# Performance work log

Measured on AMD Instinct MI355X. Metric: run time of the kernel, lower is better.

Reference implementation:

```python
import jax, jax.numpy as jnp
import numpy as np

B = 4          # number of prefill sequences (uniform cu_seqlens)
S = 1024       # tokens per sequence; total_tokens = B*S
SCALE = 0.08838834764831845  # head_dim ** -0.5


def setup_inputs() -> dict:
    key = jax.random.key(0)
    k1, k2, k3 = jax.random.split(key, 3)
    N, H, Hk, D = B * S, 16, 4, 128
    q = jax.random.normal(k1, (N, H, D), dtype=jnp.float32)
    k = jax.random.normal(k2, (N, Hk, D), dtype=jnp.float32)
    v = jax.random.normal(k3, (N, Hk, D), dtype=jnp.float32)
    k_cache = jnp.zeros((N, Hk * D), dtype=jnp.float32)
    v_cache = jnp.zeros((N, Hk * D), dtype=jnp.float32)
    slot_mapping = jnp.arange(N, dtype=jnp.int32)
    return {"q": q, "k": k, "v": v, "k_cache": k_cache,
            "v_cache": v_cache, "slot_mapping": slot_mapping}


def _store_kvcache(k, v, k_cache, v_cache, slot_mapping):
    # scatter token KV into flat paged cache; slot == -1 means skip
    N = k.shape[0]
    valid = slot_mapping >= 0
    slot = jnp.where(valid, slot_mapping, 0)
    k_flat = k.reshape(N, -1)
    v_flat = v.reshape(N, -1)
    kc = k_cache.at[slot].set(jnp.where(valid[:, None], k_flat, k_cache[slot]))
    vc = v_cache.at[slot].set(jnp.where(valid[:, None], v_flat, v_cache[slot]))
    return kc, vc


def _varlen_causal_attn(q, k, v):
    # q: [N, H, D], k/v: [N, Hk, D] with N = B*S uniform sequences (GQA)
    N, H, D = q.shape
    Hk = k.shape[1]
    G = H // Hk
    qb = q.reshape(B, S, Hk, G, D)
    kb = k.reshape(B, S, Hk, D)
    vb = v.reshape(B, S, Hk, D)
    # scores: [B, Hk, G, Sq, Sk]
    scores = jnp.einsum("bqhgd,bkhd->bhgqk", qb, kb) * jnp.float32(SCALE)
    causal = jnp.tril(jnp.ones((S, S), dtype=bool))  # [Sq, Sk]
    scores = jnp.where(causal, scores, jnp.float32(-1e30))
    p = jax.nn.softmax(scores, axis=-1)
    o = jnp.einsum("bhgqk,bkhd->bqhgd", p, vb)
    return o.reshape(N, H, D)


def reference(q, k, v, k_cache, v_cache, slot_mapping):
    kc, vc = _store_kvcache(k, v, k_cache, v_cache, slot_mapping)
    o = _varlen_causal_attn(q, k, v)
    return o, kc, vc
```

## Files before the change

kernel.cpp:

```cpp
#include <hip/hip_runtime.h>

typedef short bf16x8 __attribute__((ext_vector_type(8)));
typedef short bf16x4 __attribute__((ext_vector_type(4)));
typedef float f32x4 __attribute__((ext_vector_type(4)));

#define NB 4
#define SS 1024
#define NH 16
#define NHK 4
#define DD 128
#define NT 16
#define QSCALE 0.08838834764831845f
#define LOG2E 1.4426950408889634f

#define SB0() __builtin_amdgcn_sched_barrier(0)

__device__ __forceinline__ float exp2v(float x) { return __builtin_amdgcn_exp2f(x); }

__device__ __forceinline__ short f2bf(float f) {
  unsigned u = __builtin_bit_cast(unsigned, f);
  u += 0x7fffu + ((u >> 16) & 1u);
  return (short)(u >> 16);
}
__device__ __forceinline__ unsigned pk2(float lo, float hi) {
  return ((unsigned)(unsigned short)f2bf(hi) << 16) | (unsigned)(unsigned short)f2bf(lo);
}

typedef __attribute__((address_space(1))) const unsigned gu32;
typedef __attribute__((address_space(3))) unsigned lu32;
__device__ __forceinline__ void gload16(const void* g, void* l) {
  __builtin_amdgcn_global_load_lds((gu32*)g, (lu32*)l, 16, 0, 0);
}

__global__ __launch_bounds__(256) void scatter_kv_kernel(
    const float* __restrict__ k, const float* __restrict__ v,
    const int* __restrict__ slot, float* __restrict__ ko, float* __restrict__ vo) {
  int gid = blockIdx.x * blockDim.x + threadIdx.x;
  int tok = gid >> 7;
  int j = gid & 127;
  int s = slot[tok];
  if (s < 0) return;
  ((float4*)(ko + (size_t)s * 512))[j] = ((const float4*)(k + (size_t)tok * 512))[j];
  ((float4*)(vo + (size_t)s * 512))[j] = ((const float4*)(v + (size_t)tok * 512))[j];
}

__global__ __launch_bounds__(256) void prep_kernel(
    const float* __restrict__ k, const float* __restrict__ v,
    const int* __restrict__ slot,
    short* __restrict__ kimg, short* __restrict__ vimg,
    float* __restrict__ ko, float* __restrict__ vo) {
  __shared__ float lvf[64 * 129];
  const int blk = blockIdx.x;
  const int t = blk & 15;
  const int hk = (blk >> 4) & 3;
  const int b = blk >> 6;
  const long tb = (long)b * SS + t * 64;
  const int tid = threadIdx.x;
  short* ki = kimg + (size_t)blk * 8192;
  short* vi = vimg + (size_t)blk * 8192;

#pragma unroll
  for (int p = 0; p < 4; ++p) {
    int c = p * 256 + tid;
    int byte0 = c * 16;
    int row = byte0 >> 8;
    int d0 = (byte0 & 255) >> 1;
    const float* src = k + ((tb + row) * NHK + hk) * DD + d0;
    float4 x = *(const float4*)src;
    float4 y = *(const float4*)(src + 4);
    uint4 pk = {pk2(x.x, x.y), pk2(x.z, x.w), pk2(y.x, y.y), pk2(y.z, y.w)};
    *(uint4*)((char*)ki + (byte0 ^ ((row & 7) << 4))) = pk;
    const float* vs = v + ((tb + row) * NHK + hk) * DD + d0;
    float4 vx = *(const float4*)vs;
    float4 vy = *(const float4*)(vs + 4);
    int sl = slot[tb + row];
    if (sl >= 0) {
      float* kd = ko + (size_t)sl * 512 + hk * 128 + d0;
      *(float4*)kd = x; *(float4*)(kd + 4) = y;
      float* vd = vo + (size_t)sl * 512 + hk * 128 + d0;
      *(float4*)vd = vx; *(float4*)(vd + 4) = vy;
    }
    float* dst = &lvf[row * 129 + d0];
    dst[0] = vx.x; dst[1] = vx.y; dst[2] = vx.z; dst[3] = vx.w;
    dst[4] = vy.x; dst[5] = vy.y; dst[6] = vy.z; dst[7] = vy.w;
  }
  __syncthreads();
#pragma unroll
  for (int p = 0; p < 4; ++p) {
    int c16 = p * 256 + tid;
    int d = c16 >> 3;
    int c8 = c16 & 7;
    int pos0 = c8 * 8;
    int cblk = pos0 >> 5;
    int lg = (pos0 >> 3) & 3;
    int kvb = cblk * 32 + lg * 4;
    float f[8];
#pragma unroll
    for (int j = 0; j < 4; ++j) f[j] = lvf[(kvb + j) * 129 + d];
#pragma unroll
    for (int j = 0; j < 4; ++j) f[4 + j] = lvf[(kvb + 16 + j) * 129 + d];
    uint4 pk = {pk2(f[0], f[1]), pk2(f[2], f[3]), pk2(f[4], f[5]), pk2(f[6], f[7])};
    int byte0 = (d << 7) + (c8 << 4);
    *(uint4*)((char*)vi + (byte0 ^ ((d & 7) << 4))) = pk;
  }
}

__global__ __launch_bounds__(256, 3) void attn_kernel(
    const float* __restrict__ q, const short* __restrict__ kimg,
    const short* __restrict__ vimg, float* __restrict__ o) {
  __shared__ __align__(16) short lk[2][64 * 128];
  __shared__ __align__(16) short lv[64 * 128];

  const int tid = threadIdx.x;
  const int l = tid & 63;
  const int w = tid >> 6;
  const int lg = l >> 4;
  const int lr = l & 15;

  const int bid = blockIdx.x;
  const int x = bid & 7;
  const int s_ = bid >> 3;
  const int g = x + ((s_ >> 6) << 3);
  const int i = s_ & 63;
  const int hk = g & 3;
  const int b = g >> 2;
  const int h = hk * 4 + (i >> 4);
  const int qt = 15 - (i & 15);

  const int q_seq = qt * 64 + w * 16 + lr;
  const long qtok = (long)b * SS + q_seq;

  bf16x8 qf[4];
  {
    const float sc = QSCALE * LOG2E;
    const float* qrow = q + (qtok * NH + h) * DD;
#pragma unroll
    for (int c = 0; c < 4; ++c) {
      int d0 = c * 32 + lg * 8;
      float4 a = *(const float4*)(qrow + d0);
      float4 bb = *(const float4*)(qrow + d0 + 4);
      bf16x8 t;
      t[0] = f2bf(a.x * sc); t[1] = f2bf(a.y * sc);
      t[2] = f2bf(a.z * sc); t[3] = f2bf(a.w * sc);
      t[4] = f2bf(bb.x * sc); t[5] = f2bf(bb.y * sc);
      t[6] = f2bf(bb.z * sc); t[7] = f2bf(bb.w * sc);
      qf[c] = t;
    }
  }

  f32x4 oacc[8];
#pragma unroll
  for (int i2 = 0; i2 < 8; ++i2) oacc[i2] = f32x4{0.f, 0.f, 0.f, 0.f};
  float lsum = 0.f;

  const char* kbase = (const char*)(kimg + ((size_t)(b * NHK + hk) * NT) * 8192);
  const char* vbase = (const char*)(vimg + ((size_t)(b * NHK + hk) * NT) * 8192);

#define STAGE_K(buf, tt)                                              \
  {                                                                   \
    const char* ks_ = kbase + (size_t)(tt) * 16384;                   \
    _Pragma("unroll") for (int p4 = 0; p4 < 4; ++p4) {                \
      int off = p4 * 4096 + tid * 16;                                 \
      gload16(ks_ + off, (char*)lk + (buf) * 16384 + off);            \
    }                                                                 \
  }
#define STAGE_V(tt)                                                   \
  {                                                                   \
    const char* vs_ = vbase + (size_t)(tt) * 16384;                   \
    _Pragma("unroll") for (int p4 = 0; p4 < 4; ++p4) {                \
      int off = p4 * 4096 + tid * 16;                                 \
      gload16(vs_ + off, (char*)lv + off);                            \
    }                                                                 \
  }

  SB0();
  STAGE_K(0, 0);
  SB0();
  STAGE_V(0);
  SB0();

  for (int t = 0; t <= qt; ++t) {
    if (t < qt) {
      STAGE_K((t + 1) & 1, t + 1);
      SB0();
    }

    if (t < qt) { asm volatile("s_waitcnt vmcnt(8)" ::: "memory"); }
    else        { asm volatile("s_waitcnt vmcnt(4)" ::: "memory"); }
    SB0();
    __builtin_amdgcn_s_barrier();
    SB0();

    const char* lkc = (const char*)lk[t & 1];

    f32x4 s[4];
#pragma unroll
    for (int kt = 0; kt < 4; ++kt) {
      int row = kt * 16 + lr;
      int rb = row << 8;
      int sw = (row & 7) << 4;
      bf16x8 kf0 = *(const bf16x8*)(lkc + rb + ((0 << 6 | lg << 4) ^ sw));
      bf16x8 kf1 = *(const bf16x8*)(lkc + rb + ((1 << 6 | lg << 4) ^ sw));
      bf16x8 kf2 = *(const bf16x8*)(lkc + rb + ((2 << 6 | lg << 4) ^ sw));
      bf16x8 kf3 = *(const bf16x8*)(lkc + rb + ((3 << 6 | lg << 4) ^ sw));
      f32x4 acc = f32x4{0.f, 0.f, 0.f, 0.f};
      acc = __builtin_amdgcn_mfma_f32_16x16x32_bf16(kf0, qf[0], acc, 0, 0, 0);
      acc = __builtin_amdgcn_mfma_f32_16x16x32_bf16(kf1, qf[1], acc, 0, 0, 0);
      acc = __builtin_amdgcn_mfma_f32_16x16x32_bf16(kf2, qf[2], acc, 0, 0, 0);
      acc = __builtin_amdgcn_mfma_f32_16x16x32_bf16(kf3, qf[3], acc, 0, 0, 0);
      s[kt] = acc;
    }

    if (t == qt) {
#pragma unroll
      for (int kt = 0; kt < 4; ++kt)
#pragma unroll
        for (int r = 0; r < 4; ++r) {
          int kvg = t * 64 + kt * 16 + lg * 4 + r;
          if (kvg > q_seq) s[kt][r] = -1e30f;
        }
    }

    {
      float acc = 0.f;
#pragma unroll
      for (int kt = 0; kt < 4; ++kt)
#pragma unroll
        for (int r = 0; r < 4; ++r) {
          float pp = exp2v(s[kt][r]);
          s[kt][r] = pp;
          acc += pp;
        }
      lsum += acc;
    }

    if (t < qt) { asm volatile("s_waitcnt vmcnt(4)" ::: "memory"); }
    else        { asm volatile("s_waitcnt vmcnt(0)" ::: "memory"); }
    SB0();
    __builtin_amdgcn_s_barrier();
    SB0();

#pragma unroll
    for (int c = 0; c < 2; ++c) {
      unsigned w0, w1, w2, w3;
      asm("v_cvt_pk_bf16_f32 %0, %1, %2" : "=v"(w0) : "v"(s[2 * c][0]), "v"(s[2 * c][1]));
      asm("v_cvt_pk_bf16_f32 %0, %1, %2" : "=v"(w1) : "v"(s[2 * c][2]), "v"(s[2 * c][3]));
      asm("v_cvt_pk_bf16_f32 %0, %1, %2" : "=v"(w2) : "v"(s[2 * c + 1][0]), "v"(s[2 * c + 1][1]));
      asm("v_cvt_pk_bf16_f32 %0, %1, %2" : "=v"(w3) : "v"(s[2 * c + 1][2]), "v"(s[2 * c + 1][3]));
      union { uint4 u; bf16x8 v8; } pu;
      pu.u = uint4{w0, w1, w2, w3};
      bf16x8 pa = pu.v8;
#pragma unroll
      for (int dt = 0; dt < 8; ++dt) {
        int d = dt * 16 + lr;
        int byte = (d << 7) + (((c << 6) | (lg << 4)) ^ ((d & 7) << 4));
        bf16x8 vf = *(const bf16x8*)((const char*)lv + byte);
        oacc[dt] = __builtin_amdgcn_mfma_f32_16x16x32_bf16(pa, vf, oacc[dt], 0, 0, 0);
      }
    }

    if (t < qt) {
      SB0();
      __builtin_amdgcn_s_barrier();
      SB0();
      STAGE_V(t + 1);
      SB0();
    }
  }
#undef STAGE_K
#undef STAGE_V

  lsum += __shfl_xor(lsum, 16);
  lsum += __shfl_xor(lsum, 32);
#pragma unroll
  for (int r = 0; r < 4; ++r) {
    float inv = 1.f / __shfl(lsum, (lg << 2) + r);
    long tok = (long)b * SS + qt * 64 + w * 16 + lg * 4 + r;
    float* dst = o + (tok * NH + h) * DD + lr;
#pragma unroll
    for (int dt = 0; dt < 8; ++dt) dst[dt * 16] = oacc[dt][r] * inv;
  }
}

__global__ __launch_bounds__(256) void attn_fallback(
    const float* __restrict__ q, const float* __restrict__ k,
    const float* __restrict__ v, float* __restrict__ o) {
  __shared__ short lk[64 * 128];
  __shared__ short lvt[128 * 64];
  const int tid = threadIdx.x;
  const int l = tid & 63;
  const int w = tid >> 6;
  const int lg = l >> 4;
  const int lr = l & 15;
  const int bid = blockIdx.x;
  const int qt = bid & 15;
  const int h = (bid >> 4) & 15;
  const int b = bid >> 8;
  const int hk = h >> 2;
  const int q_seq = qt * 64 + w * 16 + lr;
  const long qtok = (long)b * SS + q_seq;
  bf16x8 qf[4];
  {
    const float* qrow = q + (qtok * NH + h) * DD;
#pragma unroll
    for (int c = 0; c < 4; ++c) {
      int d0 = c * 32 + lg * 8;
      float4 a = *(const float4*)(qrow + d0);
      float4 bb = *(const float4*)(qrow + d0 + 4);
      bf16x8 t;
      t[0] = f2bf(a.x * QSCALE); t[1] = f2bf(a.y * QSCALE);
      t[2] = f2bf(a.z * QSCALE); t[3] = f2bf(a.w * QSCALE);
      t[4] = f2bf(bb.x * QSCALE); t[5] = f2bf(bb.y * QSCALE);
      t[6] = f2bf(bb.z * QSCALE); t[7] = f2bf(bb.w * QSCALE);
      qf[c] = t;
    }
  }
  f32x4 oacc[8];
#pragma unroll
  for (int i = 0; i < 8; ++i) oacc[i] = f32x4{0.f, 0.f, 0.f, 0.f};
  float m_run = -1e30f, l_run = 0.f;
  const int ntiles = qt + 1;
  for (int t = 0; t < ntiles; ++t) {
    const long tb = (long)b * SS + t * 64;
#pragma unroll
    for (int it = 0; it < 8; ++it) {
      int task = it * 256 + tid;
      int row = task >> 5;
      int dq = (task & 31) << 2;
      float4 xx = *(const float4*)(k + ((tb + row) * NHK + hk) * DD + dq);
      int byte = (row << 8) + (dq << 1);
      byte ^= (row & 7) << 4;
      *(uint2*)((char*)lk + byte) = make_uint2(pk2(xx.x, xx.y), pk2(xx.z, xx.w));
    }
    {
      int a = tid >> 3;
      int e = tid & 7;
      const float* v0r = v + ((tb + 2 * a) * NHK + hk) * DD;
      const float* v1r = v0r + NHK * DD;
#pragma unroll
      for (int i = 0; i < 4; ++i) {
        int d0 = e * 4 + i * 32;
        float4 x0 = *(const float4*)(v0r + d0);
        float4 x1 = *(const float4*)(v1r + d0);
        unsigned pw[4] = {pk2(x0.x, x1.x), pk2(x0.y, x1.y), pk2(x0.z, x1.z), pk2(x0.w, x1.w)};
#pragma unroll
        for (int j = 0; j < 4; ++j) {
          int row = d0 + j;
          int byte = (row << 7) + (a << 2);
          byte ^= (row & 7) << 4;
          *(unsigned*)((char*)lvt + byte) = pw[j];
        }
      }
    }
    __syncthreads();
    f32x4 s[4];
#pragma unroll
    for (int kt = 0; kt < 4; ++kt) {
      f32x4 acc = f32x4{0.f, 0.f, 0.f, 0.f};
      int row = kt * 16 + lr;
#pragma unroll
      for (int c = 0; c < 4; ++c) {
        int byte = (row << 8) + (c << 6) + (lg << 4);
        byte ^= (row & 7) << 4;
        bf16x8 kf = *(const bf16x8*)((const char*)lk + byte);
        acc = __builtin_amdgcn_mfma_f32_16x16x32_bf16(kf, qf[c], acc, 0, 0, 0);
      }
      s[kt] = acc;
    }
    if (t == qt) {
#pragma unroll
      for (int kt = 0; kt < 4; ++kt)
#pragma unroll
        for (int r = 0; r < 4; ++r) {
          int kvg = t * 64 + kt * 16 + lg * 4 + r;
          if (kvg > q_seq) s[kt][r] = -1e30f;
        }
    }
    float mx = -1e30f;
#pragma unroll
    for (int kt = 0; kt < 4; ++kt)
#pragma unroll
      for (int r = 0; r < 4; ++r) mx = fmaxf(mx, s[kt][r]);
    mx = fmaxf(mx, __shfl_xor(mx, 16));
    mx = fmaxf(mx, __shfl_xor(mx, 32));
    float mnew = fmaxf(m_run, mx);
    float resc = expf(m_run - mnew);
    float rsum = 0.f;
#pragma unroll
    for (int kt = 0; kt < 4; ++kt)
#pragma unroll
      for (int r = 0; r < 4; ++r) {
        float pp = expf(s[kt][r] - mnew);
        s[kt][r] = pp;
        rsum += pp;
      }
    rsum += __shfl_xor(rsum, 16);
    rsum += __shfl_xor(rsum, 32);
    l_run = l_run * resc + rsum;
    m_run = mnew;
#pragma unroll
    for (int r = 0; r < 4; ++r) {
      float fr = __shfl(resc, (lg << 2) + r);
#pragma unroll
      for (int dt = 0; dt < 8; ++dt) oacc[dt][r] *= fr;
    }
#pragma unroll
    for (int c = 0; c < 2; ++c) {
      bf16x8 pa;
#pragma unroll
      for (int r = 0; r < 4; ++r) {
        pa[r] = f2bf(s[2 * c][r]);
        pa[r + 4] = f2bf(s[2 * c + 1][r]);
      }
#pragma unroll
      for (int dt = 0; dt < 8; ++dt) {
        int d = dt * 16 + lr;
        int rowbase = d << 7;
        int sw = (d & 7) << 4;
        int b0 = rowbase + (((c << 6) + (lg << 3)) ^ sw);
        int b1 = rowbase + (((c << 6) + 32 + (lg << 3)) ^ sw);
        bf16x4 lo = *(const bf16x4*)((const char*)lvt + b0);
        bf16x4 hi = *(const bf16x4*)((const char*)lvt + b1);
        bf16x8 vf = __builtin_shufflevector(lo, hi, 0, 1, 2, 3, 4, 5, 6, 7);
        oacc[dt] = __builtin_amdgcn_mfma_f32_16x16x32_bf16(pa, vf, oacc[dt], 0, 0, 0);
      }
    }
    __syncthreads();
  }
#pragma unroll
  for (int r = 0; r < 4; ++r) {
    float inv = 1.f / __shfl(l_run, (lg << 2) + r);
    long tok = (long)b * SS + qt * 64 + w * 16 + lg * 4 + r;
    float* dst = o + (tok * NH + h) * DD + lr;
#pragma unroll
    for (int dt = 0; dt < 8; ++dt) dst[dt * 16] = oacc[dt][r] * inv;
  }
}

extern "C" void kernel_launch(void* const* d_in, const int* in_sizes, int n_in,
                              void* d_out, int out_size, void* d_ws, size_t ws_size,
                              hipStream_t stream) {
  const float* q = (const float*)d_in[0];
  const float* k = (const float*)d_in[1];
  const float* v = (const float*)d_in[2];
  const int* slot = (const int*)d_in[5];

  float* out = (float*)d_out;
  float* o_out = out;
  float* k_out = out + (size_t)NB * SS * NH * DD;
  float* v_out = k_out + (size_t)NB * SS * NHK * DD;

  const size_t img_elems = (size_t)NB * NHK * NT * 8192;
  const size_t ws_need = img_elems * 2 * sizeof(short);

  if (ws_size >= ws_need) {
    short* kimg = (short*)d_ws;
    short* vimg = kimg + img_elems;
    prep_kernel<<<NB * NHK * NT, 256, 0, stream>>>(k, v, slot, kimg, vimg, k_out, v_out);
    attn_kernel<<<NB * NH * NT, 256, 0, stream>>>(q, kimg, vimg, o_out);
  } else {
    attn_fallback<<<NB * NH * (SS / 64), 256, 0, stream>>>(q, k, v, o_out);
    scatter_kv_kernel<<<(NB * SS * 128) / 256, 256, 0, stream>>>(k, v, slot, k_out, v_out);
  }
}
```

Baseline: 51.30 us.

## Use 128-row query tiles with 8 waves and double-buffered K/V staging

The attention kernel now runs 512-thread blocks that each own a 128-query tile (8 waves), so every K/V tile loaded into LDS is reused by twice as many queries. V also gets a double buffer, and K and V are staged together with one full drain and __syncthreads per iteration, replacing the finer vmcnt-based waits. The grid is halved, and blocks are paired across halves to balance the causal work. The risks are fewer blocks in flight and a coarser synchronisation that may expose load latency, plus per-wave causal masking on the diagonal tiles.

```diff
diff --git a/kernel.cpp b/kernel.cpp
--- a/kernel.cpp
+++ b/kernel.cpp
@@ -13,8 +13,6 @@
 #define QSCALE 0.08838834764831845f
 #define LOG2E 1.4426950408889634f
 
-#define SB0() __builtin_amdgcn_sched_barrier(0)
-
 __device__ __forceinline__ float exp2v(float x) { return __builtin_amdgcn_exp2f(x); }
 
 __device__ __forceinline__ short f2bf(float f) {
@@ -31,6 +29,12 @@
 __device__ __forceinline__ void gload16(const void* g, void* l) {
   __builtin_amdgcn_global_load_lds((gu32*)g, (lu32*)l, 16, 0, 0);
 }
+
+#define DRAIN_DMA()                                    \
+  do {                                                 \
+    asm volatile("s_waitcnt vmcnt(0)" ::: "memory");   \
+    __builtin_amdgcn_sched_barrier(0);                 \
+  } while (0)
 
 __global__ __launch_bounds__(256) void scatter_kv_kernel(
     const float* __restrict__ k, const float* __restrict__ v,
@@ -105,11 +109,11 @@
   }
 }
 
-__global__ __launch_bounds__(256, 3) void attn_kernel(
+__global__ __launch_bounds__(512, 4) void attn_kernel(
     const float* __restrict__ q, const short* __restrict__ kimg,
     const short* __restrict__ vimg, float* __restrict__ o) {
   __shared__ __align__(16) short lk[2][64 * 128];
-  __shared__ __align__(16) short lv[64 * 128];
+  __shared__ __align__(16) short lv[2][64 * 128];
 
   const int tid = threadIdx.x;
   const int l = tid & 63;
@@ -120,14 +124,19 @@
   const int bid = blockIdx.x;
   const int x = bid & 7;
   const int s_ = bid >> 3;
-  const int g = x + ((s_ >> 6) << 3);
-  const int i = s_ & 63;
-  const int hk = g & 3;
-  const int b = g >> 2;
-  const int h = hk * 4 + (i >> 4);
-  const int qt = 15 - (i & 15);
-
-  const int q_seq = qt * 64 + w * 16 + lr;
+  const int half = s_ >> 5;
+  const int i = s_ & 31;
+  const int g16 = x + (half << 3);
+  const int hk = g16 & 3;
+  const int b = g16 >> 2;
+  const int h = hk * 4 + (i >> 3);
+  const int jj0 = i & 7;
+  const int jj = half ? jj0 : 7 - jj0;
+
+  const int qbase = jj << 7;
+  const int tlast = 2 * jj + 1;
+
+  const int q_seq = qbase + w * 16 + lr;
   const long qtok = (long)b * SS + q_seq;
 
   bf16x8 qf[4];
@@ -153,45 +162,30 @@
   for (int i2 = 0; i2 < 8; ++i2) oacc[i2] = f32x4{0.f, 0.f, 0.f, 0.f};
   float lsum = 0.f;
 
-  const char* kbase = (const char*)(kimg + ((size_t)(b * NHK + hk) * NT) * 8192);
-  const char* vbase = (const char*)(vimg + ((size_t)(b * NHK + hk) * NT) * 8192);
-
-#define STAGE_K(buf, tt)                                              \
+  const char* kbase = (const char*)(kimg + ((size_t)g16 * NT) * 8192);
+  const char* vbase = (const char*)(vimg + ((size_t)g16 * NT) * 8192);
+
+#define STAGE(buf, tt)                                                \
   {                                                                   \
     const char* ks_ = kbase + (size_t)(tt) * 16384;                   \
-    _Pragma("unroll") for (int p4 = 0; p4 < 4; ++p4) {                \
-      int off = p4 * 4096 + tid * 16;                                 \
+    const char* vs_ = vbase + (size_t)(tt) * 16384;                   \
+    _Pragma("unroll") for (int p4 = 0; p4 < 2; ++p4) {                \
+      int off = p4 * 8192 + tid * 16;                                 \
       gload16(ks_ + off, (char*)lk + (buf) * 16384 + off);            \
+      gload16(vs_ + off, (char*)lv + (buf) * 16384 + off);            \
     }                                                                 \
   }
-#define STAGE_V(tt)                                                   \
-  {                                                                   \
-    const char* vs_ = vbase + (size_t)(tt) * 16384;                   \
-    _Pragma("unroll") for (int p4 = 0; p4 < 4; ++p4) {                \
-      int off = p4 * 4096 + tid * 16;                                 \
-      gload16(vs_ + off, (char*)lv + off);                            \
-    }                                                                 \
-  }
-
-  SB0();
-  STAGE_K(0, 0);
-  SB0();
-  STAGE_V(0);
-  SB0();
-
-  for (int t = 0; t <= qt; ++t) {
-    if (t < qt) {
-      STAGE_K((t + 1) & 1, t + 1);
-      SB0();
-    }
-
-    if (t < qt) { asm volatile("s_waitcnt vmcnt(8)" ::: "memory"); }
-    else        { asm volatile("s_waitcnt vmcnt(4)" ::: "memory"); }
-    SB0();
-    __builtin_amdgcn_s_barrier();
-    SB0();
-
-    const char* lkc = (const char*)lk[t & 1];
+
+  STAGE(0, 0);
+  DRAIN_DMA();
+  __syncthreads();
+
+  for (int t = 0; t <= tlast; ++t) {
+    const int cur = t & 1;
+    if (t < tlast) STAGE(cur ^ 1, t + 1);
+
+    const char* lkc = (const char*)lk[cur];
+    const char* lvc = (const char*)lv[cur];
 
     f32x4 s[4];
 #pragma unroll
@@ -211,12 +205,12 @@
       s[kt] = acc;
     }
 
-    if (t == qt) {
+    if ((t << 6) + 63 > qbase + (w << 4)) {
 #pragma unroll
       for (int kt = 0; kt < 4; ++kt)
 #pragma unroll
         for (int r = 0; r < 4; ++r) {
-          int kvg = t * 64 + kt * 16 + lg * 4 + r;
+          int kvg = (t << 6) + kt * 16 + lg * 4 + r;
           if (kvg > q_seq) s[kt][r] = -1e30f;
         }
     }
@@ -233,12 +227,6 @@
         }
       lsum += acc;
     }
-
-    if (t < qt) { asm volatile("s_waitcnt vmcnt(4)" ::: "memory"); }
-    else        { asm volatile("s_waitcnt vmcnt(0)" ::: "memory"); }
-    SB0();
-    __builtin_amdgcn_s_barrier();
-    SB0();
 
 #pragma unroll
     for (int c = 0; c < 2; ++c) {
@@ -254,28 +242,22 @@
       for (int dt = 0; dt < 8; ++dt) {
         int d = dt * 16 + lr;
         int byte = (d << 7) + (((c << 6) | (lg << 4)) ^ ((d & 7) << 4));
-        bf16x8 vf = *(const bf16x8*)((const char*)lv + byte);
+        bf16x8 vf = *(const bf16x8*)(lvc + byte);
         oacc[dt] = __builtin_amdgcn_mfma_f32_16x16x32_bf16(pa, vf, oacc[dt], 0, 0, 0);
       }
     }
 
-    if (t < qt) {
-      SB0();
-      __builtin_amdgcn_s_barrier();
-      SB0();
-      STAGE_V(t + 1);
-      SB0();
-    }
-  }
-#undef STAGE_K
-#undef STAGE_V
+    DRAIN_DMA();
+    __syncthreads();
+  }
+#undef STAGE
 
   lsum += __shfl_xor(lsum, 16);
   lsum += __shfl_xor(lsum, 32);
 #pragma unroll
   for (int r = 0; r < 4; ++r) {
     float inv = 1.f / __shfl(lsum, (lg << 2) + r);
-    long tok = (long)b * SS + qt * 64 + w * 16 + lg * 4 + r;
+    long tok = (long)b * SS + qbase + w * 16 + lg * 4 + r;
     float* dst = o + (tok * NH + h) * DD + lr;
 #pragma unroll
     for (int dt = 0; dt < 8; ++dt) dst[dt * 16] = oacc[dt][r] * inv;
@@ -457,7 +439,7 @@
     short* kimg = (short*)d_ws;
     short* vimg = kimg + img_elems;
     prep_kernel<<<NB * NHK * NT, 256, 0, stream>>>(k, v, slot, kimg, vimg, k_out, v_out);
-    attn_kernel<<<NB * NH * NT, 256, 0, stream>>>(q, kimg, vimg, o_out);
+    attn_kernel<<<NB * NH * 8, 512, 0, stream>>>(q, kimg, vimg, o_out);
   } else {
     attn_fallback<<<NB * NH * (SS / 64), 256, 0, stream>>>(q, k, v, o_out);
     scatter_kv_kernel<<<(NB * SS * 128) / 256, 256, 0, stream>>>(k, v, slot, k_out, v_out);
```

Result: faster. 46.90 us (-8.6%).
